# Optimization experiments

Measured on AMD Instinct MI355X. Metric: run time of the kernel, lower is better.

Reference implementation:

```python
import jax, jax.numpy as jnp
import numpy as np


def _conv1d(x, w, b, pad):
    # x: (B, Cin, L), w: (Cout, Cin, K) -> (B, Cout, L)
    y = jax.lax.conv_general_dilated(x, w, window_strides=(1,), padding=[(pad, pad)],
                                     dimension_numbers=('NCH', 'OIH', 'NCH'))
    return y + b[None, :, None]


def setup_inputs() -> dict:
    V, E, H, D, K = 4096, 128, 256, 64, 512  # vocab, embed, hidden, code_dim, num_codes
    B, L = 16, 2048
    key = jax.random.key(0)
    ks = jax.random.split(key, 17)

    def g(k, shape, fan_in):
        return (jax.random.normal(k, shape, jnp.float32) / np.sqrt(fan_in)).astype(jnp.float32)

    x = jax.random.randint(ks[0], (B, L), 0, V)
    token_emb = (jax.random.normal(ks[1], (V, E), jnp.float32) * 0.02).at[0].set(0.0)  # pad_id=0
    # encoder convs: k3, k3, k1
    ew1 = g(ks[2], (H, E, 3), E * 3); eb1 = jnp.zeros((H,), jnp.float32)
    ew2 = g(ks[3], (H, H, 3), H * 3); eb2 = jnp.zeros((H,), jnp.float32)
    ew3 = g(ks[4], (D, H, 1), H);     eb3 = jnp.zeros((D,), jnp.float32)
    # VQ codebook: uniform(-1/K, 1/K)
    codebook = jax.random.uniform(ks[5], (K, D), jnp.float32, minval=-1.0 / K, maxval=1.0 / K)
    # decoder convs: k1, k3, k1
    dw1 = g(ks[6], (H, D, 1), D);     db1 = jnp.zeros((H,), jnp.float32)
    dw2 = g(ks[7], (H, H, 3), H * 3); db2 = jnp.zeros((H,), jnp.float32)
    dw3 = g(ks[8], (E, H, 1), H);     db3 = jnp.zeros((E,), jnp.float32)
    out_w = g(ks[9], (V, E), E);      out_b = jnp.zeros((V,), jnp.float32)
    return {"x": x, "token_emb": token_emb,
            "ew1": ew1, "eb1": eb1, "ew2": ew2, "eb2": eb2, "ew3": ew3, "eb3": eb3,
            "codebook": codebook,
            "dw1": dw1, "db1": db1, "dw2": dw2, "db2": db2, "dw3": dw3, "db3": db3,
            "out_w": out_w, "out_b": out_b}


def reference(x, token_emb, ew1, eb1, ew2, eb2, ew3, eb3, codebook,
              dw1, db1, dw2, db2, dw3, db3, out_w, out_b):
    B, L = x.shape
    emb = token_emb[x]                              # (B, L, E)
    h = jnp.transpose(emb, (0, 2, 1))               # (B, E, L)
    h = jax.nn.relu(_conv1d(h, ew1, eb1, 1))
    h = jax.nn.relu(_conv1d(h, ew2, eb2, 1))
    h = _conv1d(h, ew3, eb3, 0)
    z_e = jnp.transpose(h, (0, 2, 1))               # (B, L, D)
    D = z_e.shape[-1]
    # --- Vector quantization (eval mode: no EMA update) ---
    flat = z_e.reshape(-1, D)                       # (B*L, D)
    dists = (flat ** 2).sum(1, keepdims=True) - 2.0 * flat @ codebook.T + (codebook ** 2).sum(1)[None, :]
    codes = jnp.argmin(dists, axis=1)               # (B*L,)
    z_q = codebook[codes].reshape(B, L, D)
    z_q_st = z_e + jax.lax.stop_gradient(z_q - z_e)
    commit = jnp.mean((jax.lax.stop_gradient(z_e) - z_q) ** 2)
    loss_vq = 0.1 * commit                          # VQVAE passes commitment_cost=0.1
    # --- Decoder ---
    hd = jnp.transpose(z_q_st, (0, 2, 1))           # (B, D, L)
    hd = jax.nn.relu(_conv1d(hd, dw1, db1, 0))
    hd = jax.nn.relu(_conv1d(hd, dw2, db2, 1))
    hd = jax.nn.relu(_conv1d(hd, dw3, db3, 0))
    hd = jnp.transpose(hd, (0, 2, 1))               # (B, L, E)
    logits = hd @ out_w.T + out_b                   # (B, L, V)
    return logits, loss_vq, codes.reshape(B, L)
```

## Files before the change

kernel.cpp:

```cpp
#include <hip/hip_runtime.h>

constexpr int Bb = 16, Ll = 2048, Ee = 128, Hh = 256, Dd = 64, Kc = 512, Vv = 4096;
constexpr int NN = Bb * Ll;
constexpr int LOGITS = NN * Vv;

typedef __attribute__((ext_vector_type(8))) short bf16x8;
typedef __attribute__((ext_vector_type(4))) float f32x4;

__global__ void transpose_w(const float* __restrict__ w, float* __restrict__ wt,
                            int Cout, int Cin, int KW) {
    int i = blockIdx.x * 256 + threadIdx.x;
    int total = Cout * Cin * KW;
    if (i >= total) return;
    int co  = i / (Cin * KW);
    int rem = i - co * (Cin * KW);
    int ci  = rem / KW;
    int k   = rem - ci * KW;
    wt[((size_t)(k * Cin + ci)) * Cout + co] = w[i];
}

__global__ void embed_kernel(const int* __restrict__ x,
                             const float4* __restrict__ te,
                             float4* __restrict__ out) {
    int gid = blockIdx.x * 256 + threadIdx.x;
    int n = gid >> 5;
    int c = gid & 31;
    out[gid] = te[((size_t)x[n] << 5) + c];
}

__device__ __forceinline__ unsigned short f2bf_rne(float f) {
    unsigned int u = __float_as_uint(f);
    unsigned int r = (u + 0x7fffu + ((u >> 16) & 1u)) >> 16;
    return (unsigned short)r;
}
__device__ __forceinline__ float bf2f(unsigned short h) {
    return __uint_as_float((unsigned int)h << 16);
}

template <bool LO_MID>
__global__ void split3(const float* __restrict__ in, short* __restrict__ out, int K) {
    int idx = blockIdx.x * 256 + threadIdx.x;
    int m = idx / K;
    int k = idx - m * K;
    float a = in[idx];
    unsigned short hi = f2bf_rne(a);
    unsigned short lo = f2bf_rne(a - bf2f(hi));
    size_t base = (size_t)m * (3 * K) + k;
    out[base]         = (short)hi;
    out[base + K]     = (short)(LO_MID ? lo : hi);
    out[base + 2 * K] = (short)(LO_MID ? hi : lo);
}

__device__ __forceinline__ void gload16(const void* g, void* l) {
    __builtin_amdgcn_global_load_lds(
        (const __attribute__((address_space(1))) unsigned int*)g,
        (__attribute__((address_space(3))) unsigned int*)l, 16, 0, 0);
}

template <bool RELU>
__global__ __launch_bounds__(256) void gemm_mfma(
    const short* __restrict__ A3, const short* __restrict__ B3,
    const float* __restrict__ bias, float* __restrict__ Y,
    int KK, int Nout) {
    __shared__ short As[4096];
    __shared__ short Bs[4096];

    const int tid  = threadIdx.x;
    const int lane = tid & 63;
    const int wid  = tid >> 6;
    const int ntile = Nout >> 7;
    const int tm = blockIdx.x / ntile;
    const int tn = blockIdx.x - tm * ntile;
    const int m0 = tm << 7;
    const int n0 = tn << 7;

    const int wm = wid >> 1, wn = wid & 1;
    const int lr = lane & 15;
    const int kg = lane >> 4;

    f32x4 acc[4][4];
#pragma unroll
    for (int i = 0; i < 4; ++i)
#pragma unroll
        for (int j = 0; j < 4; ++j)
#pragma unroll
            for (int q = 0; q < 4; ++q) acc[i][j][q] = 0.f;

    const short* Ag = A3 + (size_t)m0 * KK;
    const short* Bg = B3 + (size_t)n0 * KK;

    for (int k0 = 0; k0 < KK; k0 += 32) {
#pragma unroll
        for (int j = 0; j < 2; ++j) {
            const short* g = Ag + (size_t)(j * 64 + lane) * KK + k0 + wid * 8;
            short* l = As + (size_t)(wid * 128 + j * 64) * 8;
            gload16(g, l);
        }
#pragma unroll
        for (int j = 0; j < 2; ++j) {
            const short* g = Bg + (size_t)(j * 64 + lane) * KK + k0 + wid * 8;
            short* l = Bs + (size_t)(wid * 128 + j * 64) * 8;
            gload16(g, l);
        }
        __syncthreads();

        bf16x8 af[4], bfr[4];
#pragma unroll
        for (int i = 0; i < 4; ++i)
            af[i] = *reinterpret_cast<const bf16x8*>(
                &As[(size_t)(kg * 128 + wm * 64 + i * 16 + lr) * 8]);
#pragma unroll
        for (int j = 0; j < 4; ++j)
            bfr[j] = *reinterpret_cast<const bf16x8*>(
                &Bs[(size_t)(kg * 128 + wn * 64 + j * 16 + lr) * 8]);
#pragma unroll
        for (int i = 0; i < 4; ++i)
#pragma unroll
            for (int j = 0; j < 4; ++j)
                acc[i][j] = __builtin_amdgcn_mfma_f32_16x16x32_bf16(
                    af[i], bfr[j], acc[i][j], 0, 0, 0);
        __syncthreads();
    }

#pragma unroll
    for (int i = 0; i < 4; ++i) {
        int r0 = m0 + wm * 64 + i * 16 + kg * 4;
#pragma unroll
        for (int j = 0; j < 4; ++j) {
            int col = n0 + wn * 64 + j * 16 + lr;
            float bv = bias[col];
#pragma unroll
            for (int q = 0; q < 4; ++q) {
                float v = acc[i][j][q] + bv;
                if (RELU) v = fmaxf(v, 0.f);
                Y[(size_t)(r0 + q) * Nout + col] = v;
            }
        }
    }
}

template <int KW, bool RELU, int BM, int BN, int TM, int TN>
__global__ __launch_bounds__(256) void gemm_conv(
    const float* __restrict__ A, const float* __restrict__ Wt,
    const float* __restrict__ bias, float* __restrict__ Y, int Cin, int Cout) {
    constexpr int BK = 16;
    const int tid = threadIdx.x;
    const int tx = tid % (BN / TN);
    const int ty = tid / (BN / TN);
    const int n0  = blockIdx.x * BM;
    const int co0 = blockIdx.y * BN;

    __shared__ float As[BK][BM + 4];
    __shared__ float Bs[BK][BN];

    float acc[TM][TN];
#pragma unroll
    for (int i = 0; i < TM; i++)
#pragma unroll
        for (int j = 0; j < TN; j++) acc[i][j] = 0.f;

    constexpr int A4 = BM * BK / (256 * 4);
    constexpr int B4 = BN * BK / (256 * 4);

    for (int k = 0; k < KW; ++k) {
        const int shift = k - (KW - 1) / 2;
        for (int ci0 = 0; ci0 < Cin; ci0 += BK) {
#pragma unroll
            for (int v = 0; v < A4; ++v) {
                int f4 = v * 256 + tid;
                int r  = f4 / (BK / 4);
                int c4 = f4 % (BK / 4);
                int n = n0 + r;
                float4 val = make_float4(0.f, 0.f, 0.f, 0.f);
                if (KW == 1) {
                    val = *(const float4*)(A + (size_t)n * Cin + ci0 + c4 * 4);
                } else {
                    int l  = n & (Ll - 1);
                    int sl = l + shift;
                    if ((unsigned)sl < (unsigned)Ll)
                        val = *(const float4*)(A + (size_t)(n + shift) * Cin + ci0 + c4 * 4);
                }
                As[c4 * 4 + 0][r] = val.x;
                As[c4 * 4 + 1][r] = val.y;
                As[c4 * 4 + 2][r] = val.z;
                As[c4 * 4 + 3][r] = val.w;
            }
#pragma unroll
            for (int v = 0; v < B4; ++v) {
                int f4 = v * 256 + tid;
                int c  = f4 / (BN / 4);
                int j4 = f4 % (BN / 4);
                float4 w4 = *(const float4*)(Wt + (size_t)(k * Cin + ci0 + c) * Cout + co0 + j4 * 4);
                *(float4*)(&Bs[c][j4 * 4]) = w4;
            }
            __syncthreads();
#pragma unroll
            for (int cc = 0; cc < BK; ++cc) {
                float a[TM], b[TN];
#pragma unroll
                for (int i = 0; i < TM; i += 4)
                    *(float4*)(&a[i]) = *(const float4*)(&As[cc][ty * TM + i]);
#pragma unroll
                for (int j = 0; j < TN; j += 4)
                    *(float4*)(&b[j]) = *(const float4*)(&Bs[cc][tx * TN + j]);
#pragma unroll
                for (int i = 0; i < TM; i++)
#pragma unroll
                    for (int j = 0; j < TN; j++)
                        acc[i][j] = fmaf(a[i], b[j], acc[i][j]);
            }
            __syncthreads();
        }
    }
#pragma unroll
    for (int i = 0; i < TM; i++) {
        int n = n0 + ty * TM + i;
#pragma unroll
        for (int j = 0; j < TN; j += 4) {
            int co = co0 + tx * TN + j;
            float4 r;
            r.x = acc[i][j + 0] + bias[co + 0];
            r.y = acc[i][j + 1] + bias[co + 1];
            r.z = acc[i][j + 2] + bias[co + 2];
            r.w = acc[i][j + 3] + bias[co + 3];
            if (RELU) {
                r.x = fmaxf(r.x, 0.f); r.y = fmaxf(r.y, 0.f);
                r.z = fmaxf(r.z, 0.f); r.w = fmaxf(r.w, 0.f);
            }
            *(float4*)(Y + (size_t)n * Cout + co) = r;
        }
    }
}

__global__ __launch_bounds__(256) void vq_kernel(
    const float* __restrict__ ze, const float* __restrict__ cb,
    int* __restrict__ codes_i, float* __restrict__ codes_f) {
    const int tid = threadIdx.x;
    const int tx = tid & 15, ty = tid >> 4;
    const int n0 = blockIdx.x * 64;

    __shared__ float Zs[Dd][64 + 4];
    __shared__ float Cs[Dd][64 + 4];
    __shared__ float bD[64][17];
    __shared__ int   bI[64][17];

#pragma unroll
    for (int v = 0; v < 4; ++v) {
        int f4 = v * 256 + tid;
        int row = f4 >> 4, d4 = f4 & 15;
        float4 z = *(const float4*)(ze + (size_t)(n0 + row) * Dd + d4 * 4);
        Zs[d4 * 4 + 0][row] = z.x;
        Zs[d4 * 4 + 1][row] = z.y;
        Zs[d4 * 4 + 2][row] = z.z;
        Zs[d4 * 4 + 3][row] = z.w;
    }

    float best[4];
    int   bidx[4];
#pragma unroll
    for (int i = 0; i < 4; i++) { best[i] = 3.4e38f; bidx[i] = 0; }

    for (int ch = 0; ch < Kc / 64; ++ch) {
        int c0 = ch * 64;
        __syncthreads();
#pragma unroll
        for (int v = 0; v < 4; ++v) {
            int f4 = v * 256 + tid;
            int j = f4 >> 4, d4 = f4 & 15;
            float4 w = *(const float4*)(cb + (size_t)(c0 + j) * Dd + d4 * 4);
            Cs[d4 * 4 + 0][j] = w.x;
            Cs[d4 * 4 + 1][j] = w.y;
            Cs[d4 * 4 + 2][j] = w.z;
            Cs[d4 * 4 + 3][j] = w.w;
        }
        __syncthreads();

        float dist[4][4];
#pragma unroll
        for (int i = 0; i < 4; i++)
#pragma unroll
            for (int j = 0; j < 4; j++) dist[i][j] = 0.f;

#pragma unroll 8
        for (int d = 0; d < Dd; ++d) {
            float a[4], b[4];
            *(float4*)a = *(const float4*)(&Zs[d][ty * 4]);
            *(float4*)b = *(const float4*)(&Cs[d][tx * 4]);
#pragma unroll
            for (int i = 0; i < 4; i++)
#pragma unroll
                for (int j = 0; j < 4; j++) {
                    float df = a[i] - b[j];
                    dist[i][j] = fmaf(df, df, dist[i][j]);
                }
        }
#pragma unroll
        for (int i = 0; i < 4; i++)
#pragma unroll
            for (int j = 0; j < 4; j++) {
                int ci = c0 + tx * 4 + j;
                if (dist[i][j] < best[i]) { best[i] = dist[i][j]; bidx[i] = ci; }
            }
    }
    __syncthreads();
#pragma unroll
    for (int i = 0; i < 4; i++) {
        bD[ty * 4 + i][tx] = best[i];
        bI[ty * 4 + i][tx] = bidx[i];
    }
    __syncthreads();
    if (tid < 64) {
        float bd = bD[tid][0];
        int   bi = bI[tid][0];
        for (int t = 1; t < 16; ++t) {
            float d = bD[tid][t];
            int   ix = bI[tid][t];
            if (d < bd || (d == bd && ix < bi)) { bd = d; bi = ix; }
        }
        codes_i[n0 + tid] = bi;
        codes_f[n0 + tid] = (float)bi;
    }
}

__global__ void gather_zq(const int* __restrict__ codes,
                          const float4* __restrict__ cb, float4* __restrict__ zq) {
    int gid = blockIdx.x * 256 + threadIdx.x;
    int n = gid >> 4, c = gid & 15;
    zq[gid] = cb[((size_t)codes[n] << 4) + c];
}

__global__ __launch_bounds__(256) void commit_partial(
    const float* __restrict__ ze, const float* __restrict__ zq,
    float* __restrict__ partial) {
    float s = 0.f;
    for (int i = blockIdx.x * 256 + threadIdx.x; i < NN * Dd; i += 1024 * 256) {
        float d = ze[i] - zq[i];
        s = fmaf(d, d, s);
    }
    for (int off = 32; off; off >>= 1) s += __shfl_down(s, off, 64);
    __shared__ float w[4];
    int lane = threadIdx.x & 63, wv = threadIdx.x >> 6;
    if (lane == 0) w[wv] = s;
    __syncthreads();
    if (threadIdx.x == 0) partial[blockIdx.x] = w[0] + w[1] + w[2] + w[3];
}

__global__ void commit_final(const float* __restrict__ partial, float* __restrict__ loss) {
    float s = 0.f;
    for (int i = threadIdx.x; i < 1024; i += 256) s += partial[i];
    for (int off = 32; off; off >>= 1) s += __shfl_down(s, off, 64);
    __shared__ float w[4];
    int lane = threadIdx.x & 63, wv = threadIdx.x >> 6;
    if (lane == 0) w[wv] = s;
    __syncthreads();
    if (threadIdx.x == 0)
        loss[0] = 0.1f * (w[0] + w[1] + w[2] + w[3]) / (float)(NN * Dd);
}

extern "C" void kernel_launch(void* const* d_in, const int* in_sizes, int n_in,
                              void* d_out, int out_size, void* d_ws, size_t ws_size,
                              hipStream_t stream) {
    const int*   x    = (const int*)d_in[0];
    const float* te   = (const float*)d_in[1];
    const float* ew1  = (const float*)d_in[2];
    const float* eb1  = (const float*)d_in[3];
    const float* ew2  = (const float*)d_in[4];
    const float* eb2  = (const float*)d_in[5];
    const float* ew3  = (const float*)d_in[6];
    const float* eb3  = (const float*)d_in[7];
    const float* cb   = (const float*)d_in[8];
    const float* dw1  = (const float*)d_in[9];
    const float* db1  = (const float*)d_in[10];
    const float* dw2  = (const float*)d_in[11];
    const float* db2  = (const float*)d_in[12];
    const float* dw3  = (const float*)d_in[13];
    const float* db3  = (const float*)d_in[14];
    const float* outw = (const float*)d_in[15];
    const float* outb = (const float*)d_in[16];

    char* ws = (char*)d_ws;
    size_t off = 0;
    auto alloc = [&](size_t bytes) -> void* {
        void* p = ws + off;
        off = (off + bytes + 255) & ~(size_t)255;
        return p;
    };
    float* bufA   = (float*)alloc((size_t)NN * Ee * 4);
    float* bufB   = (float*)alloc((size_t)NN * Hh * 4);
    float* bufC   = (float*)alloc((size_t)NN * Hh * 4);
    float* bufZ   = (float*)alloc((size_t)NN * Dd * 4);
    float* bufQ   = (float*)alloc((size_t)NN * Dd * 4);
    int*   codesi = (int*)alloc((size_t)NN * 4);
    float* part   = (float*)alloc(1024 * 4);
    float* wt_e1  = (float*)alloc((size_t)3 * Ee * Hh * 4);
    float* wt_e2  = (float*)alloc((size_t)3 * Hh * Hh * 4);
    float* wt_e3  = (float*)alloc((size_t)Hh * Dd * 4);
    float* wt_d1  = (float*)alloc((size_t)Dd * Hh * 4);
    float* wt_d2  = (float*)alloc((size_t)3 * Hh * Hh * 4);
    float* wt_d3  = (float*)alloc((size_t)Hh * Ee * 4);
    short* a3     = (short*)alloc((size_t)NN * 3 * Ee * 2);
    short* w3     = (short*)alloc((size_t)Vv * 3 * Ee * 2);

    float* out       = (float*)d_out;
    float* out_loss  = out + (size_t)LOGITS;
    float* out_codes = out_loss + 1;

    auto tg = [](int n) { return dim3((n + 255) / 256); };
    transpose_w<<<tg(Hh * Ee * 3), 256, 0, stream>>>(ew1, wt_e1, Hh, Ee, 3);
    transpose_w<<<tg(Hh * Hh * 3), 256, 0, stream>>>(ew2, wt_e2, Hh, Hh, 3);
    transpose_w<<<tg(Dd * Hh),     256, 0, stream>>>(ew3, wt_e3, Dd, Hh, 1);
    transpose_w<<<tg(Hh * Dd),     256, 0, stream>>>(dw1, wt_d1, Hh, Dd, 1);
    transpose_w<<<tg(Hh * Hh * 3), 256, 0, stream>>>(dw2, wt_d2, Hh, Hh, 3);
    transpose_w<<<tg(Ee * Hh),     256, 0, stream>>>(dw3, wt_d3, Ee, Hh, 1);
    split3<false><<<tg(Vv * Ee), 256, 0, stream>>>(outw, w3, Ee);

    embed_kernel<<<dim3(NN * 32 / 256), 256, 0, stream>>>(x, (const float4*)te, (float4*)bufA);

    gemm_conv<3, true, 128, 128, 8, 8><<<dim3(NN / 128, Hh / 128), 256, 0, stream>>>(bufA, wt_e1, eb1, bufB, Ee, Hh);
    gemm_conv<3, true, 128, 128, 8, 8><<<dim3(NN / 128, Hh / 128), 256, 0, stream>>>(bufB, wt_e2, eb2, bufC, Hh, Hh);
    gemm_conv<1, false, 64, 64, 4, 4><<<dim3(NN / 64, 1), 256, 0, stream>>>(bufC, wt_e3, eb3, bufZ, Hh, Dd);

    vq_kernel<<<dim3(NN / 64), 256, 0, stream>>>(bufZ, cb, codesi, out_codes);
    gather_zq<<<dim3(NN * 16 / 256), 256, 0, stream>>>(codesi, (const float4*)cb, (float4*)bufQ);
    commit_partial<<<dim3(1024), 256, 0, stream>>>(bufZ, bufQ, part);
    commit_final<<<dim3(1), 256, 0, stream>>>(part, out_loss);

    gemm_conv<1, true, 128, 128, 8, 8><<<dim3(NN / 128, Hh / 128), 256, 0, stream>>>(bufQ, wt_d1, db1, bufB, Dd, Hh);
    gemm_conv<3, true, 128, 128, 8, 8><<<dim3(NN / 128, Hh / 128), 256, 0, stream>>>(bufB, wt_d2, db2, bufC, Hh, Hh);
    gemm_conv<1, true, 128, 128, 8, 8><<<dim3(NN / 128, Ee / 128), 256, 0, stream>>>(bufC, wt_d3, db3, bufA, Hh, Ee);

    split3<true><<<tg(NN * Ee), 256, 0, stream>>>(bufA, a3, Ee);
    gemm_mfma<false><<<dim3((NN / 128) * (Vv / 128)), 256, 0, stream>>>(
        a3, w3, outb, out, 3 * Ee, Vv);
}
```

Baseline: 1.292 ms.

## Move decoder convolutions onto split-bf16 MFMA GEMMs with fused split epilogue

The three decoder convolutions move from the fp32 SIMT gemm_conv kernel to the bf16 MFMA GEMM, using a three-term hi/lo bf16 split to keep near-fp32 accuracy. The k=3 conv is handled inside the GEMM through shifted row loads, with a zeroed guard row standing in for padding. Each layer's epilogue writes the next layer's split bf16 format directly, so the separate split pass is no longer needed. The patch also adds a block-index swizzle for L2 locality and split-codebook gathering, at the cost of extra preprocessing launches and bf16-split precision in the decoder.

```diff
diff --git a/kernel.cpp b/kernel.cpp
--- a/kernel.cpp
+++ b/kernel.cpp
@@ -51,26 +51,58 @@
     out[base + 2 * K] = (short)(LO_MID ? hi : lo);
 }
 
+__global__ void split3_w3(const float* __restrict__ w, short* __restrict__ w3,
+                          int Cout, int Cin) {
+    int idx = blockIdx.x * 256 + threadIdx.x;
+    int total = Cout * Cin * 3;
+    if (idx >= total) return;
+    int co  = idx / (Cin * 3);
+    int rem = idx - co * (Cin * 3);
+    int ci  = rem / 3;
+    int k   = rem - ci * 3;
+    float a = w[idx];
+    unsigned short hi = f2bf_rne(a);
+    unsigned short lo = f2bf_rne(a - bf2f(hi));
+    size_t base = (size_t)co * (9 * Cin) + (size_t)k * (3 * Cin) + ci;
+    w3[base]            = (short)hi;
+    w3[base + Cin]      = (short)hi;
+    w3[base + 2 * Cin]  = (short)lo;
+}
+
+__global__ void zero_guards(short* __restrict__ q3, short* __restrict__ h1,
+                            short* __restrict__ h2, short* __restrict__ h3) {
+    int t = threadIdx.x;
+    for (int i = t; i < 192; i += 256) q3[(size_t)NN * 192 + i] = 0;
+    for (int i = t; i < 768; i += 256) h1[(size_t)NN * 768 + i] = 0;
+    for (int i = t; i < 768; i += 256) h2[(size_t)NN * 768 + i] = 0;
+    for (int i = t; i < 384; i += 256) h3[(size_t)NN * 384 + i] = 0;
+}
+
 __device__ __forceinline__ void gload16(const void* g, void* l) {
     __builtin_amdgcn_global_load_lds(
         (const __attribute__((address_space(1))) unsigned int*)g,
         (__attribute__((address_space(3))) unsigned int*)l, 16, 0, 0);
 }
 
-template <bool RELU>
+template <int KW, bool RELU, bool OUT3>
 __global__ __launch_bounds__(256) void gemm_mfma(
     const short* __restrict__ A3, const short* __restrict__ B3,
-    const float* __restrict__ bias, float* __restrict__ Y,
-    int KK, int Nout) {
+    const float* __restrict__ bias, float* __restrict__ Yf,
+    short* __restrict__ Y3, int KK, int Nout) {
     __shared__ short As[4096];
     __shared__ short Bs[4096];
 
     const int tid  = threadIdx.x;
     const int lane = tid & 63;
     const int wid  = tid >> 6;
+
+    const int nwg = gridDim.x;
+    const int bid = blockIdx.x;
+    const int swz = (bid & 7) * (nwg >> 3) + (bid >> 3);
+
     const int ntile = Nout >> 7;
-    const int tm = blockIdx.x / ntile;
-    const int tn = blockIdx.x - tm * ntile;
+    const int tm = swz / ntile;
+    const int tn = swz - tm * ntile;
     const int m0 = tm << 7;
     const int n0 = tn << 7;
 
@@ -86,40 +118,49 @@
 #pragma unroll
             for (int q = 0; q < 4; ++q) acc[i][j][q] = 0.f;
 
-    const short* Ag = A3 + (size_t)m0 * KK;
-    const short* Bg = B3 + (size_t)n0 * KK;
-
-    for (int k0 = 0; k0 < KK; k0 += 32) {
-#pragma unroll
-        for (int j = 0; j < 2; ++j) {
-            const short* g = Ag + (size_t)(j * 64 + lane) * KK + k0 + wid * 8;
-            short* l = As + (size_t)(wid * 128 + j * 64) * 8;
-            gload16(g, l);
-        }
-#pragma unroll
-        for (int j = 0; j < 2; ++j) {
-            const short* g = Bg + (size_t)(j * 64 + lane) * KK + k0 + wid * 8;
-            short* l = Bs + (size_t)(wid * 128 + j * 64) * 8;
-            gload16(g, l);
-        }
-        __syncthreads();
-
-        bf16x8 af[4], bfr[4];
-#pragma unroll
-        for (int i = 0; i < 4; ++i)
-            af[i] = *reinterpret_cast<const bf16x8*>(
-                &As[(size_t)(kg * 128 + wm * 64 + i * 16 + lr) * 8]);
-#pragma unroll
-        for (int j = 0; j < 4; ++j)
-            bfr[j] = *reinterpret_cast<const bf16x8*>(
-                &Bs[(size_t)(kg * 128 + wn * 64 + j * 16 + lr) * 8]);
-#pragma unroll
-        for (int i = 0; i < 4; ++i)
+    const int BKW = KW * KK;
+
+    for (int kt = 0; kt < KW; ++kt) {
+        const int shift = kt - (KW - 1) / 2;
+        for (int k0 = 0; k0 < KK; k0 += 32) {
+#pragma unroll
+            for (int j = 0; j < 2; ++j) {
+                int r = m0 + j * 64 + lane;
+                int src = r;
+                if (KW > 1) {
+                    int sl = (r & (Ll - 1)) + shift;
+                    src = ((unsigned)sl < (unsigned)Ll) ? r + shift : NN;
+                }
+                const short* g = A3 + (size_t)src * KK + k0 + wid * 8;
+                short* l = As + (size_t)(wid * 128 + j * 64) * 8;
+                gload16(g, l);
+            }
+#pragma unroll
+            for (int j = 0; j < 2; ++j) {
+                const short* g = B3 + (size_t)(n0 + j * 64 + lane) * BKW
+                                 + kt * KK + k0 + wid * 8;
+                short* l = Bs + (size_t)(wid * 128 + j * 64) * 8;
+                gload16(g, l);
+            }
+            __syncthreads();
+
+            bf16x8 af[4], bfr[4];
+#pragma unroll
+            for (int i = 0; i < 4; ++i)
+                af[i] = *reinterpret_cast<const bf16x8*>(
+                    &As[(size_t)(kg * 128 + wm * 64 + i * 16 + lr) * 8]);
 #pragma unroll
             for (int j = 0; j < 4; ++j)
-                acc[i][j] = __builtin_amdgcn_mfma_f32_16x16x32_bf16(
-                    af[i], bfr[j], acc[i][j], 0, 0, 0);
-        __syncthreads();
+                bfr[j] = *reinterpret_cast<const bf16x8*>(
+                    &Bs[(size_t)(kg * 128 + wn * 64 + j * 16 + lr) * 8]);
+#pragma unroll
+            for (int i = 0; i < 4; ++i)
+#pragma unroll
+                for (int j = 0; j < 4; ++j)
+                    acc[i][j] = __builtin_amdgcn_mfma_f32_16x16x32_bf16(
+                        af[i], bfr[j], acc[i][j], 0, 0, 0);
+            __syncthreads();
+        }
     }
 
 #pragma unroll
@@ -133,7 +174,16 @@
             for (int q = 0; q < 4; ++q) {
                 float v = acc[i][j][q] + bv;
                 if (RELU) v = fmaxf(v, 0.f);
-                Y[(size_t)(r0 + q) * Nout + col] = v;
+                if (OUT3) {
+                    unsigned short hi = f2bf_rne(v);
+                    unsigned short lo = f2bf_rne(v - bf2f(hi));
+                    size_t rb = (size_t)(r0 + q) * (3 * Nout);
+                    Y3[rb + col]            = (short)hi;
+                    Y3[rb + Nout + col]     = (short)lo;
+                    Y3[rb + 2 * Nout + col] = (short)hi;
+                } else {
+                    Yf[(size_t)(r0 + q) * Nout + col] = v;
+                }
             }
         }
     }
@@ -327,6 +377,13 @@
     int gid = blockIdx.x * 256 + threadIdx.x;
     int n = gid >> 4, c = gid & 15;
     zq[gid] = cb[((size_t)codes[n] << 4) + c];
+}
+
+__global__ void gather_q3(const int* __restrict__ codes,
+                          const float4* __restrict__ cb3, float4* __restrict__ q3) {
+    int gid = blockIdx.x * 256 + threadIdx.x;
+    int n = gid / 24, c = gid - n * 24;
+    q3[(size_t)n * 24 + c] = cb3[(size_t)codes[n] * 24 + c];
 }
 
 __global__ __launch_bounds__(256) void commit_partial(
@@ -395,11 +452,15 @@
     float* wt_e1  = (float*)alloc((size_t)3 * Ee * Hh * 4);
     float* wt_e2  = (float*)alloc((size_t)3 * Hh * Hh * 4);
     float* wt_e3  = (float*)alloc((size_t)Hh * Dd * 4);
-    float* wt_d1  = (float*)alloc((size_t)Dd * Hh * 4);
-    float* wt_d2  = (float*)alloc((size_t)3 * Hh * Hh * 4);
-    float* wt_d3  = (float*)alloc((size_t)Hh * Ee * 4);
-    short* a3     = (short*)alloc((size_t)NN * 3 * Ee * 2);
-    short* w3     = (short*)alloc((size_t)Vv * 3 * Ee * 2);
+    short* cb3    = (short*)alloc((size_t)Kc * 3 * Dd * 2);
+    short* q3     = (short*)alloc((size_t)(NN + 1) * 3 * Dd * 2);
+    short* h1_3   = (short*)alloc((size_t)(NN + 1) * 3 * Hh * 2);
+    short* h2_3   = (short*)alloc((size_t)(NN + 1) * 3 * Hh * 2);
+    short* h3_3   = (short*)alloc((size_t)(NN + 1) * 3 * Ee * 2);
+    short* wd1_3  = (short*)alloc((size_t)Hh * 3 * Dd * 2);
+    short* wd2_3  = (short*)alloc((size_t)Hh * 9 * Hh * 2);
+    short* wd3_3  = (short*)alloc((size_t)Ee * 3 * Hh * 2);
+    short* wo3    = (short*)alloc((size_t)Vv * 3 * Ee * 2);
 
     float* out       = (float*)d_out;
     float* out_loss  = out + (size_t)LOGITS;
@@ -409,10 +470,12 @@
     transpose_w<<<tg(Hh * Ee * 3), 256, 0, stream>>>(ew1, wt_e1, Hh, Ee, 3);
     transpose_w<<<tg(Hh * Hh * 3), 256, 0, stream>>>(ew2, wt_e2, Hh, Hh, 3);
     transpose_w<<<tg(Dd * Hh),     256, 0, stream>>>(ew3, wt_e3, Dd, Hh, 1);
-    transpose_w<<<tg(Hh * Dd),     256, 0, stream>>>(dw1, wt_d1, Hh, Dd, 1);
-    transpose_w<<<tg(Hh * Hh * 3), 256, 0, stream>>>(dw2, wt_d2, Hh, Hh, 3);
-    transpose_w<<<tg(Ee * Hh),     256, 0, stream>>>(dw3, wt_d3, Ee, Hh, 1);
-    split3<false><<<tg(Vv * Ee), 256, 0, stream>>>(outw, w3, Ee);
+    split3<false><<<tg(Hh * Dd),  256, 0, stream>>>(dw1, wd1_3, Dd);
+    split3_w3<<<tg(Hh * Hh * 3),  256, 0, stream>>>(dw2, wd2_3, Hh, Hh);
+    split3<false><<<tg(Ee * Hh),  256, 0, stream>>>(dw3, wd3_3, Hh);
+    split3<false><<<tg(Vv * Ee),  256, 0, stream>>>(outw, wo3, Ee);
+    split3<true><<<tg(Kc * Dd),   256, 0, stream>>>(cb, cb3, Dd);
+    zero_guards<<<dim3(1), 256, 0, stream>>>(q3, h1_3, h2_3, h3_3);
 
     embed_kernel<<<dim3(NN * 32 / 256), 256, 0, stream>>>(x, (const float4*)te, (float4*)bufA);
 
@@ -422,14 +485,17 @@
 
     vq_kernel<<<dim3(NN / 64), 256, 0, stream>>>(bufZ, cb, codesi, out_codes);
     gather_zq<<<dim3(NN * 16 / 256), 256, 0, stream>>>(codesi, (const float4*)cb, (float4*)bufQ);
+    gather_q3<<<tg(NN * 24), 256, 0, stream>>>(codesi, (const float4*)cb3, (float4*)q3);
     commit_partial<<<dim3(1024), 256, 0, stream>>>(bufZ, bufQ, part);
     commit_final<<<dim3(1), 256, 0, stream>>>(part, out_loss);
 
-    gemm_conv<1, true, 128, 128, 8, 8><<<dim3(NN / 128, Hh / 128), 256, 0, stream>>>(bufQ, wt_d1, db1, bufB, Dd, Hh);
-    gemm_conv<3, true, 128, 128, 8, 8><<<dim3(NN / 128, Hh / 128), 256, 0, stream>>>(bufB, wt_d2, db2, bufC, Hh, Hh);
-    gemm_conv<1, true, 128, 128, 8, 8><<<dim3(NN / 128, Ee / 128), 256, 0, stream>>>(bufC, wt_d3, db3, bufA, Hh, Ee);
-
-    split3<true><<<tg(NN * Ee), 256, 0, stream>>>(bufA, a3, Ee);
-    gemm_mfma<false><<<dim3((NN / 128) * (Vv / 128)), 256, 0, stream>>>(
-        a3, w3, outb, out, 3 * Ee, Vv);
-}
+    gemm_mfma<1, true, true><<<dim3((NN / 128) * (Hh / 128)), 256, 0, stream>>>(
+        q3, wd1_3, db1, nullptr, h1_3, 3 * Dd, Hh);
+    gemm_mfma<3, true, true><<<dim3((NN / 128) * (Hh / 128)), 256, 0, stream>>>(
+        h1_3, wd2_3, db2, nullptr, h2_3, 3 * Hh, Hh);
+    gemm_mfma<1, true, true><<<dim3((NN / 128) * (Ee / 128)), 256, 0, stream>>>(
+        h2_3, wd3_3, db3, nullptr, h3_3, 3 * Hh, Ee);
+
+    gemm_mfma<1, false, false><<<dim3((NN / 128) * (Vv / 128)), 256, 0, stream>>>(
+        h3_3, wo3, outb, out, nullptr, 3 * Ee, Vv);
+}
```

Result: faster. 1.224 ms (-5.3%).

## Run all convolutions on bf16 MFMA with split-precision operands and gathered inputs

Applied to the files above, without the earlier changes.

Replaces the fp32 FMA convolution kernels with the bf16 MFMA GEMM, extended for kernel-width-3 shifts, row gathers (embedding and codebook lookups) and epilogues that directly emit split bf16 hi/lo (or three-term) operand layouts for the next layer. Weight transposes and splits are merged into a single prep kernel, and the embed, gather_zq and split3 kernels are removed by gathering inside the GEMM. A grouped block swizzle is added to the GEMM. This targets the dominant fp32 SIMT conv cost, but makes accuracy depend on multi-term bf16 emulation, notably in the encoder feeding the argmin.

```diff
diff --git a/kernel.cpp b/kernel.cpp
--- a/kernel.cpp
+++ b/kernel.cpp
@@ -7,49 +7,139 @@
 typedef __attribute__((ext_vector_type(8))) short bf16x8;
 typedef __attribute__((ext_vector_type(4))) float f32x4;
 
-__global__ void transpose_w(const float* __restrict__ w, float* __restrict__ wt,
-                            int Cout, int Cin, int KW) {
-    int i = blockIdx.x * 256 + threadIdx.x;
-    int total = Cout * Cin * KW;
-    if (i >= total) return;
-    int co  = i / (Cin * KW);
-    int rem = i - co * (Cin * KW);
-    int ci  = rem / KW;
-    int k   = rem - ci * KW;
-    wt[((size_t)(k * Cin + ci)) * Cout + co] = w[i];
-}
-
-__global__ void embed_kernel(const int* __restrict__ x,
-                             const float4* __restrict__ te,
-                             float4* __restrict__ out) {
-    int gid = blockIdx.x * 256 + threadIdx.x;
-    int n = gid >> 5;
-    int c = gid & 31;
-    out[gid] = te[((size_t)x[n] << 5) + c];
-}
-
 __device__ __forceinline__ unsigned short f2bf_rne(float f) {
     unsigned int u = __float_as_uint(f);
-    unsigned int r = (u + 0x7fffu + ((u >> 16) & 1u)) >> 16;
-    return (unsigned short)r;
+    return (unsigned short)((u + 0x7fffu + ((u >> 16) & 1u)) >> 16);
 }
 __device__ __forceinline__ float bf2f(unsigned short h) {
     return __uint_as_float((unsigned int)h << 16);
 }
-
-template <bool LO_MID>
-__global__ void split3(const float* __restrict__ in, short* __restrict__ out, int K) {
-    int idx = blockIdx.x * 256 + threadIdx.x;
-    int m = idx / K;
-    int k = idx - m * K;
-    float a = in[idx];
-    unsigned short hi = f2bf_rne(a);
-    unsigned short lo = f2bf_rne(a - bf2f(hi));
-    size_t base = (size_t)m * (3 * K) + k;
-    out[base]         = (short)hi;
-    out[base + K]     = (short)(LO_MID ? lo : hi);
-    out[base + 2 * K] = (short)(LO_MID ? hi : lo);
-}
+__device__ __forceinline__ void split3f(float v, unsigned short& a1,
+                                        unsigned short& a2, unsigned short& a3) {
+    a1 = f2bf_rne(v);
+    float r = v - bf2f(a1);
+    a2 = f2bf_rne(r);
+    r -= bf2f(a2);
+    a3 = f2bf_rne(r);
+}
+
+__global__ __launch_bounds__(256) void prep(
+    const float* __restrict__ te,  const float* __restrict__ ew1,
+    const float* __restrict__ ew2, const float* __restrict__ ew3,
+    const float* __restrict__ eb3, const float* __restrict__ dw1,
+    const float* __restrict__ dw2, const float* __restrict__ dw3,
+    const float* __restrict__ outw, const float* __restrict__ cb,
+    short* __restrict__ te6, short* __restrict__ we1, short* __restrict__ we2,
+    short* __restrict__ we3, float* __restrict__ eb3p,
+    short* __restrict__ wd1, short* __restrict__ wd2, short* __restrict__ wd3,
+    short* __restrict__ wo3, short* __restrict__ cb3,
+    short* __restrict__ h1_6, short* __restrict__ h1_3) {
+    int id = blockIdx.x * 256 + threadIdx.x;
+    unsigned short a1, a2, a3;
+    if (id < (Vv + 1) * Ee) {
+        int t = id / Ee, c = id - t * Ee;
+        size_t rb = (size_t)t * 768;
+        if (t == Vv) {
+            te6[rb + c] = 0; te6[rb + 128 + c] = 0; te6[rb + 256 + c] = 0;
+            te6[rb + 384 + c] = 0; te6[rb + 512 + c] = 0; te6[rb + 640 + c] = 0;
+            return;
+        }
+        split3f(te[(size_t)t * Ee + c], a1, a2, a3);
+        te6[rb + c] = (short)a1;       te6[rb + 128 + c] = (short)a1;
+        te6[rb + 256 + c] = (short)a2; te6[rb + 384 + c] = (short)a1;
+        te6[rb + 512 + c] = (short)a2; te6[rb + 640 + c] = (short)a3;
+        return;
+    }
+    id -= (Vv + 1) * Ee;
+    if (id < Hh * Ee * 3) {
+        int co = id / (Ee * 3); int rem = id - co * (Ee * 3);
+        int ci = rem / 3, k = rem - ci * 3;
+        split3f(ew1[id], a1, a2, a3);
+        size_t b = (size_t)co * 2304 + (size_t)k * 768 + ci;
+        we1[b] = (short)a1;       we1[b + 128] = (short)a2;
+        we1[b + 256] = (short)a1; we1[b + 384] = (short)a3;
+        we1[b + 512] = (short)a2; we1[b + 640] = (short)a1;
+        return;
+    }
+    id -= Hh * Ee * 3;
+    if (id < Hh * Hh * 3) {
+        int co = id / (Hh * 3); int rem = id - co * (Hh * 3);
+        int ci = rem / 3, k = rem - ci * 3;
+        split3f(ew2[id], a1, a2, a3);
+        size_t b = (size_t)co * 4608 + (size_t)k * 1536 + ci;
+        we2[b] = (short)a1;        we2[b + 256] = (short)a2;
+        we2[b + 512] = (short)a1;  we2[b + 768] = (short)a3;
+        we2[b + 1024] = (short)a2; we2[b + 1280] = (short)a1;
+        return;
+    }
+    id -= Hh * Hh * 3;
+    if (id < Dd * Hh) {
+        int co = id / Hh, ci = id - co * Hh;
+        split3f(ew3[id], a1, a2, a3);
+        size_t b = (size_t)co * 1536 + ci;
+        we3[b] = (short)a1;        we3[b + 256] = (short)a2;
+        we3[b + 512] = (short)a1;  we3[b + 768] = (short)a3;
+        we3[b + 1024] = (short)a2; we3[b + 1280] = (short)a1;
+        return;
+    }
+    id -= Dd * Hh;
+    if (id < 64 * 1536) { we3[(size_t)64 * 1536 + id] = 0; return; }
+    id -= 64 * 1536;
+    if (id < Hh * Dd) {
+        int co = id / Dd, ci = id - co * Dd;
+        float v = dw1[id];
+        unsigned short hi = f2bf_rne(v), lo = f2bf_rne(v - bf2f(hi));
+        size_t b = (size_t)co * 192 + ci;
+        wd1[b] = (short)hi; wd1[b + 64] = (short)hi; wd1[b + 128] = (short)lo;
+        return;
+    }
+    id -= Hh * Dd;
+    if (id < Hh * Hh * 3) {
+        int co = id / (Hh * 3); int rem = id - co * (Hh * 3);
+        int ci = rem / 3, k = rem - ci * 3;
+        float v = dw2[id];
+        unsigned short hi = f2bf_rne(v), lo = f2bf_rne(v - bf2f(hi));
+        size_t b = (size_t)co * 2304 + (size_t)k * 768 + ci;
+        wd2[b] = (short)hi; wd2[b + 256] = (short)hi; wd2[b + 512] = (short)lo;
+        return;
+    }
+    id -= Hh * Hh * 3;
+    if (id < Ee * Hh) {
+        int co = id / Hh, ci = id - co * Hh;
+        float v = dw3[id];
+        unsigned short hi = f2bf_rne(v), lo = f2bf_rne(v - bf2f(hi));
+        size_t b = (size_t)co * 768 + ci;
+        wd3[b] = (short)hi; wd3[b + 256] = (short)hi; wd3[b + 512] = (short)lo;
+        return;
+    }
+    id -= Ee * Hh;
+    if (id < Vv * Ee) {
+        int co = id / Ee, ci = id - co * Ee;
+        float v = outw[id];
+        unsigned short hi = f2bf_rne(v), lo = f2bf_rne(v - bf2f(hi));
+        size_t b = (size_t)co * 384 + ci;
+        wo3[b] = (short)hi; wo3[b + 128] = (short)hi; wo3[b + 256] = (short)lo;
+        return;
+    }
+    id -= Vv * Ee;
+    if (id < Kc * Dd) {
+        int n = id / Dd, c = id - n * Dd;
+        float v = cb[id];
+        unsigned short hi = f2bf_rne(v), lo = f2bf_rne(v - bf2f(hi));
+        size_t b = (size_t)n * 192 + c;
+        cb3[b] = (short)hi; cb3[b + 64] = (short)lo; cb3[b + 128] = (short)hi;
+        return;
+    }
+    id -= Kc * Dd;
+    if (id < 1536) { h1_6[(size_t)NN * 1536 + id] = 0; return; }
+    id -= 1536;
+    if (id < 768)  { h1_3[(size_t)NN * 768 + id] = 0; return; }
+    id -= 768;
+    if (id < 128)  { eb3p[id] = (id < Dd) ? eb3[id] : 0.f; return; }
+}
+constexpr int PREP_TOTAL = (Vv + 1) * Ee + Hh * Ee * 3 + Hh * Hh * 3 + Dd * Hh
+    + 64 * 1536 + Hh * Dd + Hh * Hh * 3 + Ee * Hh + Vv * Ee + Kc * Dd
+    + 1536 + 768 + 128;
 
 __device__ __forceinline__ void gload16(const void* g, void* l) {
     __builtin_amdgcn_global_load_lds(
@@ -57,20 +147,25 @@
         (__attribute__((address_space(3))) unsigned int*)l, 16, 0, 0);
 }
 
-template <bool RELU>
+template <int KW, bool RELU, int OMODE, bool GATHER>
 __global__ __launch_bounds__(256) void gemm_mfma(
-    const short* __restrict__ A3, const short* __restrict__ B3,
-    const float* __restrict__ bias, float* __restrict__ Y,
-    int KK, int Nout) {
+    const short* __restrict__ A3, const int* __restrict__ idx, int guard,
+    const short* __restrict__ B3, const float* __restrict__ bias,
+    float* __restrict__ Yf, short* __restrict__ Y3, int KK, int Nout) {
     __shared__ short As[4096];
     __shared__ short Bs[4096];
 
     const int tid  = threadIdx.x;
     const int lane = tid & 63;
     const int wid  = tid >> 6;
+
+    const int nwg = gridDim.x;
+    const int bid = blockIdx.x;
+    const int swz = (bid & 7) * (nwg >> 3) + (bid >> 3);
+
     const int ntile = Nout >> 7;
-    const int tm = blockIdx.x / ntile;
-    const int tn = blockIdx.x - tm * ntile;
+    const int tm = swz / ntile;
+    const int tn = swz - tm * ntile;
     const int m0 = tm << 7;
     const int n0 = tn << 7;
 
@@ -86,40 +181,53 @@
 #pragma unroll
             for (int q = 0; q < 4; ++q) acc[i][j][q] = 0.f;
 
-    const short* Ag = A3 + (size_t)m0 * KK;
-    const short* Bg = B3 + (size_t)n0 * KK;
-
-    for (int k0 = 0; k0 < KK; k0 += 32) {
+    const int BKW = KW * KK;
+
+    for (int kt = 0; kt < KW; ++kt) {
+        const int shift = kt - (KW - 1) / 2;
+        size_t arow[2];
 #pragma unroll
         for (int j = 0; j < 2; ++j) {
-            const short* g = Ag + (size_t)(j * 64 + lane) * KK + k0 + wid * 8;
-            short* l = As + (size_t)(wid * 128 + j * 64) * 8;
-            gload16(g, l);
-        }
-#pragma unroll
-        for (int j = 0; j < 2; ++j) {
-            const short* g = Bg + (size_t)(j * 64 + lane) * KK + k0 + wid * 8;
-            short* l = Bs + (size_t)(wid * 128 + j * 64) * 8;
-            gload16(g, l);
-        }
-        __syncthreads();
-
-        bf16x8 af[4], bfr[4];
-#pragma unroll
-        for (int i = 0; i < 4; ++i)
-            af[i] = *reinterpret_cast<const bf16x8*>(
-                &As[(size_t)(kg * 128 + wm * 64 + i * 16 + lr) * 8]);
-#pragma unroll
-        for (int j = 0; j < 4; ++j)
-            bfr[j] = *reinterpret_cast<const bf16x8*>(
-                &Bs[(size_t)(kg * 128 + wn * 64 + j * 16 + lr) * 8]);
-#pragma unroll
-        for (int i = 0; i < 4; ++i)
+            int n = m0 + j * 64 + lane;
+            int src;
+            if (KW > 1) {
+                int sl = (n & (Ll - 1)) + shift;
+                bool valid = (unsigned)sl < (unsigned)Ll;
+                if (GATHER) src = valid ? idx[n + shift] : guard;
+                else        src = valid ? n + shift : guard;
+            } else {
+                src = GATHER ? idx[n] : n;
+            }
+            arow[j] = (size_t)src * KK;
+        }
+        for (int k0 = 0; k0 < KK; k0 += 32) {
+#pragma unroll
+            for (int j = 0; j < 2; ++j)
+                gload16(A3 + arow[j] + k0 + wid * 8,
+                        As + (size_t)(wid * 128 + j * 64) * 8);
+#pragma unroll
+            for (int j = 0; j < 2; ++j)
+                gload16(B3 + (size_t)(n0 + j * 64 + lane) * BKW + kt * KK + k0 + wid * 8,
+                        Bs + (size_t)(wid * 128 + j * 64) * 8);
+            __syncthreads();
+
+            bf16x8 af[4], bfr[4];
+#pragma unroll
+            for (int i = 0; i < 4; ++i)
+                af[i] = *reinterpret_cast<const bf16x8*>(
+                    &As[(size_t)(kg * 128 + wm * 64 + i * 16 + lr) * 8]);
 #pragma unroll
             for (int j = 0; j < 4; ++j)
-                acc[i][j] = __builtin_amdgcn_mfma_f32_16x16x32_bf16(
-                    af[i], bfr[j], acc[i][j], 0, 0, 0);
-        __syncthreads();
+                bfr[j] = *reinterpret_cast<const bf16x8*>(
+                    &Bs[(size_t)(kg * 128 + wn * 64 + j * 16 + lr) * 8]);
+#pragma unroll
+            for (int i = 0; i < 4; ++i)
+#pragma unroll
+                for (int j = 0; j < 4; ++j)
+                    acc[i][j] = __builtin_amdgcn_mfma_f32_16x16x32_bf16(
+                        af[i], bfr[j], acc[i][j], 0, 0, 0);
+            __syncthreads();
+        }
     }
 
 #pragma unroll
@@ -133,101 +241,26 @@
             for (int q = 0; q < 4; ++q) {
                 float v = acc[i][j][q] + bv;
                 if (RELU) v = fmaxf(v, 0.f);
-                Y[(size_t)(r0 + q) * Nout + col] = v;
+                if (OMODE == 0) {
+                    Yf[(size_t)(r0 + q) * Nout + col] = v;
+                } else if (OMODE == 1) {
+                    unsigned short hi = f2bf_rne(v), lo = f2bf_rne(v - bf2f(hi));
+                    size_t rb = (size_t)(r0 + q) * (3 * Nout);
+                    Y3[rb + col]            = (short)hi;
+                    Y3[rb + Nout + col]     = (short)lo;
+                    Y3[rb + 2 * Nout + col] = (short)hi;
+                } else {
+                    unsigned short s1, s2, s3;
+                    split3f(v, s1, s2, s3);
+                    size_t rb = (size_t)(r0 + q) * (6 * Nout);
+                    Y3[rb + col]            = (short)s1;
+                    Y3[rb + Nout + col]     = (short)s1;
+                    Y3[rb + 2 * Nout + col] = (short)s2;
+                    Y3[rb + 3 * Nout + col] = (short)s1;
+                    Y3[rb + 4 * Nout + col] = (short)s2;
+                    Y3[rb + 5 * Nout + col] = (short)s3;
+                }
             }
-        }
-    }
-}
-
-template <int KW, bool RELU, int BM, int BN, int TM, int TN>
-__global__ __launch_bounds__(256) void gemm_conv(
-    const float* __restrict__ A, const float* __restrict__ Wt,
-    const float* __restrict__ bias, float* __restrict__ Y, int Cin, int Cout) {
-    constexpr int BK = 16;
-    const int tid = threadIdx.x;
-    const int tx = tid % (BN / TN);
-    const int ty = tid / (BN / TN);
-    const int n0  = blockIdx.x * BM;
-    const int co0 = blockIdx.y * BN;
-
-    __shared__ float As[BK][BM + 4];
-    __shared__ float Bs[BK][BN];
-
-    float acc[TM][TN];
-#pragma unroll
-    for (int i = 0; i < TM; i++)
-#pragma unroll
-        for (int j = 0; j < TN; j++) acc[i][j] = 0.f;
-
-    constexpr int A4 = BM * BK / (256 * 4);
-    constexpr int B4 = BN * BK / (256 * 4);
-
-    for (int k = 0; k < KW; ++k) {
-        const int shift = k - (KW - 1) / 2;
-        for (int ci0 = 0; ci0 < Cin; ci0 += BK) {
-#pragma unroll
-            for (int v = 0; v < A4; ++v) {
-                int f4 = v * 256 + tid;
-                int r  = f4 / (BK / 4);
-                int c4 = f4 % (BK / 4);
-                int n = n0 + r;
-                float4 val = make_float4(0.f, 0.f, 0.f, 0.f);
-                if (KW == 1) {
-                    val = *(const float4*)(A + (size_t)n * Cin + ci0 + c4 * 4);
-                } else {
-                    int l  = n & (Ll - 1);
-                    int sl = l + shift;
-                    if ((unsigned)sl < (unsigned)Ll)
-                        val = *(const float4*)(A + (size_t)(n + shift) * Cin + ci0 + c4 * 4);
-                }
-                As[c4 * 4 + 0][r] = val.x;
-                As[c4 * 4 + 1][r] = val.y;
-                As[c4 * 4 + 2][r] = val.z;
-                As[c4 * 4 + 3][r] = val.w;
-            }
-#pragma unroll
-            for (int v = 0; v < B4; ++v) {
-                int f4 = v * 256 + tid;
-                int c  = f4 / (BN / 4);
-                int j4 = f4 % (BN / 4);
-                float4 w4 = *(const float4*)(Wt + (size_t)(k * Cin + ci0 + c) * Cout + co0 + j4 * 4);
-                *(float4*)(&Bs[c][j4 * 4]) = w4;
-            }
-            __syncthreads();
-#pragma unroll
-            for (int cc = 0; cc < BK; ++cc) {
-                float a[TM], b[TN];
-#pragma unroll
-                for (int i = 0; i < TM; i += 4)
-                    *(float4*)(&a[i]) = *(const float4*)(&As[cc][ty * TM + i]);
-#pragma unroll
-                for (int j = 0; j < TN; j += 4)
-                    *(float4*)(&b[j]) = *(const float4*)(&Bs[cc][tx * TN + j]);
-#pragma unroll
-                for (int i = 0; i < TM; i++)
-#pragma unroll
-                    for (int j = 0; j < TN; j++)
-                        acc[i][j] = fmaf(a[i], b[j], acc[i][j]);
-            }
-            __syncthreads();
-        }
-    }
-#pragma unroll
-    for (int i = 0; i < TM; i++) {
-        int n = n0 + ty * TM + i;
-#pragma unroll
-        for (int j = 0; j < TN; j += 4) {
-            int co = co0 + tx * TN + j;
-            float4 r;
-            r.x = acc[i][j + 0] + bias[co + 0];
-            r.y = acc[i][j + 1] + bias[co + 1];
-            r.z = acc[i][j + 2] + bias[co + 2];
-            r.w = acc[i][j + 3] + bias[co + 3];
-            if (RELU) {
-                r.x = fmaxf(r.x, 0.f); r.y = fmaxf(r.y, 0.f);
-                r.z = fmaxf(r.z, 0.f); r.w = fmaxf(r.w, 0.f);
-            }
-            *(float4*)(Y + (size_t)n * Cout + co) = r;
         }
     }
 }
@@ -248,7 +281,7 @@
     for (int v = 0; v < 4; ++v) {
         int f4 = v * 256 + tid;
         int row = f4 >> 4, d4 = f4 & 15;
-        float4 z = *(const float4*)(ze + (size_t)(n0 + row) * Dd + d4 * 4);
+        float4 z = *(const float4*)(ze + (size_t)(n0 + row) * 128 + d4 * 4);
         Zs[d4 * 4 + 0][row] = z.x;
         Zs[d4 * 4 + 1][row] = z.y;
         Zs[d4 * 4 + 2][row] = z.z;
@@ -322,20 +355,17 @@
     }
 }
 
-__global__ void gather_zq(const int* __restrict__ codes,
-                          const float4* __restrict__ cb, float4* __restrict__ zq) {
-    int gid = blockIdx.x * 256 + threadIdx.x;
-    int n = gid >> 4, c = gid & 15;
-    zq[gid] = cb[((size_t)codes[n] << 4) + c];
-}
-
 __global__ __launch_bounds__(256) void commit_partial(
-    const float* __restrict__ ze, const float* __restrict__ zq,
-    float* __restrict__ partial) {
+    const float* __restrict__ zep, const float* __restrict__ cb,
+    const int* __restrict__ codes, float* __restrict__ partial) {
     float s = 0.f;
-    for (int i = blockIdx.x * 256 + threadIdx.x; i < NN * Dd; i += 1024 * 256) {
-        float d = ze[i] - zq[i];
-        s = fmaf(d, d, s);
+    for (int i4 = blockIdx.x * 256 + threadIdx.x; i4 < NN * 16; i4 += 1024 * 256) {
+        int n = i4 >> 4, d4 = i4 & 15;
+        float4 z = *(const float4*)(zep + (size_t)n * 128 + d4 * 4);
+        float4 c = *(const float4*)(cb + (size_t)codes[n] * Dd + d4 * 4);
+        float dx = z.x - c.x, dy = z.y - c.y, dz = z.z - c.z, dw = z.w - c.w;
+        s = fmaf(dx, dx, s); s = fmaf(dy, dy, s);
+        s = fmaf(dz, dz, s); s = fmaf(dw, dw, s);
     }
     for (int off = 32; off; off >>= 1) s += __shfl_down(s, off, 64);
     __shared__ float w[4];
@@ -385,51 +415,52 @@
         off = (off + bytes + 255) & ~(size_t)255;
         return p;
     };
-    float* bufA   = (float*)alloc((size_t)NN * Ee * 4);
-    float* bufB   = (float*)alloc((size_t)NN * Hh * 4);
-    float* bufC   = (float*)alloc((size_t)NN * Hh * 4);
-    float* bufZ   = (float*)alloc((size_t)NN * Dd * 4);
-    float* bufQ   = (float*)alloc((size_t)NN * Dd * 4);
+    short* te6    = (short*)alloc((size_t)(Vv + 1) * 768 * 2);
+    short* we1_6  = (short*)alloc((size_t)Hh * 2304 * 2);
+    short* we2_6  = (short*)alloc((size_t)Hh * 4608 * 2);
+    short* we3_6  = (short*)alloc((size_t)128 * 1536 * 2);
+    float* eb3p   = (float*)alloc(128 * 4);
+    short* h1_6   = (short*)alloc((size_t)(NN + 1) * 1536 * 2);
+    short* h2_6   = (short*)alloc((size_t)(NN + 1) * 1536 * 2);
+    float* zep    = (float*)alloc((size_t)NN * 128 * 4);
     int*   codesi = (int*)alloc((size_t)NN * 4);
     float* part   = (float*)alloc(1024 * 4);
-    float* wt_e1  = (float*)alloc((size_t)3 * Ee * Hh * 4);
-    float* wt_e2  = (float*)alloc((size_t)3 * Hh * Hh * 4);
-    float* wt_e3  = (float*)alloc((size_t)Hh * Dd * 4);
-    float* wt_d1  = (float*)alloc((size_t)Dd * Hh * 4);
-    float* wt_d2  = (float*)alloc((size_t)3 * Hh * Hh * 4);
-    float* wt_d3  = (float*)alloc((size_t)Hh * Ee * 4);
-    short* a3     = (short*)alloc((size_t)NN * 3 * Ee * 2);
-    short* w3     = (short*)alloc((size_t)Vv * 3 * Ee * 2);
+    short* cb3    = (short*)alloc((size_t)Kc * 192 * 2);
+    short* h1_3   = (short*)alloc((size_t)(NN + 1) * 768 * 2);
+    short* h2_3   = (short*)alloc((size_t)(NN + 1) * 768 * 2);
+    short* h3_3   = (short*)alloc((size_t)(NN + 1) * 384 * 2);
+    short* wd1_3  = (short*)alloc((size_t)Hh * 192 * 2);
+    short* wd2_3  = (short*)alloc((size_t)Hh * 2304 * 2);
+    short* wd3_3  = (short*)alloc((size_t)Ee * 768 * 2);
+    short* wo3    = (short*)alloc((size_t)Vv * 384 * 2);
 
     float* out       = (float*)d_out;
     float* out_loss  = out + (size_t)LOGITS;
     float* out_codes = out_loss + 1;
 
-    auto tg = [](int n) { return dim3((n + 255) / 256); };
-    transpose_w<<<tg(Hh * Ee * 3), 256, 0, stream>>>(ew1, wt_e1, Hh, Ee, 3);
-    transpose_w<<<tg(Hh * Hh * 3), 256, 0, stream>>>(ew2, wt_e2, Hh, Hh, 3);
-    transpose_w<<<tg(Dd * Hh),     256, 0, stream>>>(ew3, wt_e3, Dd, Hh, 1);
-    transpose_w<<<tg(Hh * Dd),     256, 0, stream>>>(dw1, wt_d1, Hh, Dd, 1);
-    transpose_w<<<tg(Hh * Hh * 3), 256, 0, stream>>>(dw2, wt_d2, Hh, Hh, 3);
-    transpose_w<<<tg(Ee * Hh),     256, 0, stream>>>(dw3, wt_d3, Ee, Hh, 1);
-    split3<false><<<tg(Vv * Ee), 256, 0, stream>>>(outw, w3, Ee);
-
-    embed_kernel<<<dim3(NN * 32 / 256), 256, 0, stream>>>(x, (const float4*)te, (float4*)bufA);
-
-    gemm_conv<3, true, 128, 128, 8, 8><<<dim3(NN / 128, Hh / 128), 256, 0, stream>>>(bufA, wt_e1, eb1, bufB, Ee, Hh);
-    gemm_conv<3, true, 128, 128, 8, 8><<<dim3(NN / 128, Hh / 128), 256, 0, stream>>>(bufB, wt_e2, eb2, bufC, Hh, Hh);
-    gemm_conv<1, false, 64, 64, 4, 4><<<dim3(NN / 64, 1), 256, 0, stream>>>(bufC, wt_e3, eb3, bufZ, Hh, Dd);
-
-    vq_kernel<<<dim3(NN / 64), 256, 0, stream>>>(bufZ, cb, codesi, out_codes);
-    gather_zq<<<dim3(NN * 16 / 256), 256, 0, stream>>>(codesi, (const float4*)cb, (float4*)bufQ);
-    commit_partial<<<dim3(1024), 256, 0, stream>>>(bufZ, bufQ, part);
+    prep<<<dim3((PREP_TOTAL + 255) / 256), 256, 0, stream>>>(
+        te, ew1, ew2, ew3, eb3, dw1, dw2, dw3, outw, cb,
+        te6, we1_6, we2_6, we3_6, eb3p, wd1_3, wd2_3, wd3_3, wo3, cb3,
+        h1_6, h1_3);
+
+    gemm_mfma<3, true, 2, true><<<dim3(512), 256, 0, stream>>>(
+        te6, x, Vv, we1_6, eb1, nullptr, h1_6, 768, Hh);
+    gemm_mfma<3, true, 2, false><<<dim3(512), 256, 0, stream>>>(
+        h1_6, nullptr, NN, we2_6, eb2, nullptr, h2_6, 1536, Hh);
+    gemm_mfma<1, false, 0, false><<<dim3(256), 256, 0, stream>>>(
+        h2_6, nullptr, 0, we3_6, eb3p, zep, nullptr, 1536, 128);
+
+    vq_kernel<<<dim3(NN / 64), 256, 0, stream>>>(zep, cb, codesi, out_codes);
+    commit_partial<<<dim3(1024), 256, 0, stream>>>(zep, cb, codesi, part);
     commit_final<<<dim3(1), 256, 0, stream>>>(part, out_loss);
 
-    gemm_conv<1, true, 128, 128, 8, 8><<<dim3(NN / 128, Hh / 128), 256, 0, stream>>>(bufQ, wt_d1, db1, bufB, Dd, Hh);
-    gemm_conv<3, true, 128, 128, 8, 8><<<dim3(NN / 128, Hh / 128), 256, 0, stream>>>(bufB, wt_d2, db2, bufC, Hh, Hh);
-    gemm_conv<1, true, 128, 128, 8, 8><<<dim3(NN / 128, Ee / 128), 256, 0, stream>>>(bufC, wt_d3, db3, bufA, Hh, Ee);
-
-    split3<true><<<tg(NN * Ee), 256, 0, stream>>>(bufA, a3, Ee);
-    gemm_mfma<false><<<dim3((NN / 128) * (Vv / 128)), 256, 0, stream>>>(
-        a3, w3, outb, out, 3 * Ee, Vv);
-}
+    gemm_mfma<1, true, 1, true><<<dim3(512), 256, 0, stream>>>(
+        cb3, codesi, 0, wd1_3, db1, nullptr, h1_3, 192, Hh);
+    gemm_mfma<3, true, 1, false><<<dim3(512), 256, 0, stream>>>(
+        h1_3, nullptr, NN, wd2_3, db2, nullptr, h2_3, 768, Hh);
+    gemm_mfma<1, true, 1, false><<<dim3(256), 256, 0, stream>>>(
+        h2_3, nullptr, 0, wd3_3, db3, nullptr, h3_3, 768, Ee);
+
+    gemm_mfma<1, false, 0, false><<<dim3(8192), 256, 0, stream>>>(
+        h3_3, nullptr, 0, wo3, outb, out, nullptr, 384, Vv);
+}
```

Result: no change. 1.276 ms (-1.3%).
